# Optimization experiments

Measured on AMD Instinct MI355X. Metric: run time of the kernel, lower is better.

## Reference

```python
import jax, jax.numpy as jnp
import numpy as np

EPS = 1e-6

def rmsnorm(x, w):
    return x * jax.lax.rsqrt(jnp.mean(x * x, axis=-1, keepdims=True) + EPS) * w

def hard_sigmoid(x):
    # relu6(x + 3) / 6 - 0.5
    return jnp.clip(x + 3.0, 0.0, 6.0) / 6.0 - 0.5

def setup_inputs() -> dict:
    key = jax.random.key(0)
    ks = jax.random.split(key, 8)
    B, T, C, E = 4, 4096, 1024, 4
    H = E * C
    x = jax.random.normal(ks[0], (B, T, C), dtype=jnp.float32)
    norm1_w = jnp.ones((C,), dtype=jnp.float32)
    norm2_w = jnp.ones((C,), dtype=jnp.float32)
    s1 = 1.0 / np.sqrt(C)
    s2 = 1.0 / np.sqrt(H)
    mlp1_w = jax.random.uniform(ks[1], (C, C), jnp.float32, -s1, s1)
    mlp1_b = jax.random.uniform(ks[2], (C,), jnp.float32, -s1, s1)
    mlp2a_w = jax.random.uniform(ks[3], (C, H), jnp.float32, -s1, s1)
    mlp2a_b = jax.random.uniform(ks[4], (H,), jnp.float32, -s1, s1)
    mlp2b_w = jax.random.uniform(ks[5], (H, C), jnp.float32, -s2, s2)
    mlp2b_b = jax.random.uniform(ks[6], (C,), jnp.float32, -s2, s2)
    return {"x": x, "norm1_w": norm1_w, "mlp1_w": mlp1_w, "mlp1_b": mlp1_b,
            "norm2_w": norm2_w, "mlp2a_w": mlp2a_w, "mlp2a_b": mlp2a_b,
            "mlp2b_w": mlp2b_w, "mlp2b_b": mlp2b_b}

def reference(x, norm1_w, mlp1_w, mlp1_b, norm2_w, mlp2a_w, mlp2a_b, mlp2b_w, mlp2b_b):
    # state: [B, T, C] prefix sum over time of gated, normalized input
    state = jnp.cumsum(hard_sigmoid(rmsnorm(x, norm1_w)), axis=1)
    out = hard_sigmoid(state @ mlp1_w + mlp1_b) * x
    h = jax.nn.relu(rmsnorm(out, norm2_w) @ mlp2a_w + mlp2a_b)
    return h @ mlp2b_w + mlp2b_b + out
```

## Files before the change

kernel.cpp:

```cpp
#include <hip/hip_runtime.h>

#define B_     4
#define T_     4096
#define C_     1024
#define H_     4096
#define BT_    (B_ * T_)
#define NCH_   64
#define CHLEN_ 64
#define MCHUNK 8192

typedef __bf16 bf16_t;
typedef __bf16 bf16x8 __attribute__((ext_vector_type(8)));
typedef float  f32x4  __attribute__((ext_vector_type(4)));

__device__ __forceinline__ float hs_f(float v) {
    return fminf(fmaxf((v + 3.0f) * (1.0f / 6.0f), 0.0f), 1.0f) - 0.5f;
}

__device__ __forceinline__ void gld_lds16(const bf16_t* g, bf16_t* l) {
    __builtin_amdgcn_global_load_lds((const __attribute__((address_space(1))) void*)g,
                                     (__attribute__((address_space(3))) void*)l,
                                     16, 0, 0);
}

__global__ __launch_bounds__(256) void rms_rows_f32(const float* __restrict__ X,
                                                    float* __restrict__ inv) {
    const int wave = threadIdx.x >> 6, lane = threadIdx.x & 63;
    const int row = blockIdx.x * 4 + wave;
    const float* xr = X + (size_t)row * C_;
    float s = 0.0f;
    #pragma unroll
    for (int p = 0; p < 4; p++) {
        float4 v = *(const float4*)(xr + p * 256 + lane * 4);
        s += v.x * v.x + v.y * v.y + v.z * v.z + v.w * v.w;
    }
    #pragma unroll
    for (int o = 32; o > 0; o >>= 1) s += __shfl_down(s, o, 64);
    if (lane == 0) inv[row] = rsqrtf(s * (1.0f / C_) + 1e-6f);
}

__global__ __launch_bounds__(256) void rms_rows_bf16(const bf16_t* __restrict__ X,
                                                     float* __restrict__ inv) {
    const int wave = threadIdx.x >> 6, lane = threadIdx.x & 63;
    const int row = blockIdx.x * 4 + wave;
    const bf16_t* xr = X + (size_t)row * C_;
    bf16x8 v0 = *(const bf16x8*)(xr + lane * 8);
    bf16x8 v1 = *(const bf16x8*)(xr + 512 + lane * 8);
    float s = 0.0f;
    #pragma unroll
    for (int j = 0; j < 8; j++) {
        float a = (float)v0[j], b = (float)v1[j];
        s += a * a + b * b;
    }
    #pragma unroll
    for (int o = 32; o > 0; o >>= 1) s += __shfl_down(s, o, 64);
    if (lane == 0) inv[row] = rsqrtf(s * (1.0f / C_) + 1e-6f);
}

__global__ __launch_bounds__(256) void scan_emit_local(const float* __restrict__ X,
                                                       const float* __restrict__ inv1,
                                                       const float* __restrict__ nw,
                                                       bf16_t* __restrict__ state,
                                                       float* __restrict__ csum) {
    const int bch = blockIdx.x;
    const int b = bch >> 6, ch = bch & 63;
    const int c = blockIdx.y * 256 + threadIdx.x;
    const float wgt = nw[c];
    const int rbase = b * T_ + ch * CHLEN_;
    const size_t xbase = (size_t)rbase * C_ + c;
    float acc = 0.0f;
    for (int i = 0; i < CHLEN_; i++) {
        acc += hs_f(X[xbase + (size_t)i * C_] * inv1[rbase + i] * wgt);
        state[(size_t)(rbase + i) * C_ + c] = (bf16_t)acc;
    }
    csum[(size_t)bch * C_ + c] = acc;
}

__global__ __launch_bounds__(256) void scan_offsets_hilo(const float* __restrict__ csum,
                                                         bf16_t* __restrict__ hilo) {
    const int idx = blockIdx.x * 256 + threadIdx.x;
    const int b = idx >> 10, c = idx & 1023;
    const size_t base = (size_t)b * NCH_ * C_ + c;
    float v[NCH_];
    #pragma unroll
    for (int ch = 0; ch < NCH_; ch++)
        v[ch] = csum[base + (size_t)ch * C_];
    float run = 0.0f;
    #pragma unroll
    for (int ch = 0; ch < NCH_; ch++) {
        const size_t row = (size_t)(b * NCH_ + ch) * 2048 + c;
        const bf16_t hi = (bf16_t)run;
        hilo[row] = hi;
        hilo[row + 1024] = (bf16_t)(run - (float)hi);
        run += v[ch];
    }
}

__global__ __launch_bounds__(256) void pmat_init(const float* __restrict__ b1,
                                                 float* __restrict__ Pmat) {
    const int i = blockIdx.x * 256 + threadIdx.x;
    Pmat[i] = b1[i & (C_ - 1)];
}

__global__ __launch_bounds__(256) void transpose_scale(const float* __restrict__ src,
                                                       bf16_t* __restrict__ dst,
                                                       int K, int N, int ldd, int dupOff,
                                                       const float* __restrict__ scale) {
    __shared__ float tile[32][33];
    const int n0 = blockIdx.x * 32, k0 = blockIdx.y * 32;
    const int tx = threadIdx.x & 31, ty = threadIdx.x >> 5;
    #pragma unroll
    for (int j = 0; j < 4; j++) {
        const int kk = ty + j * 8;
        float v = src[(size_t)(k0 + kk) * N + n0 + tx];
        if (scale) v *= scale[k0 + kk];
        tile[kk][tx] = v;
    }
    __syncthreads();
    #pragma unroll
    for (int j = 0; j < 4; j++) {
        const int nn = ty + j * 8;
        const bf16_t v = (bf16_t)tile[tx][nn];
        dst[(size_t)(n0 + nn) * ldd + k0 + tx] = v;
        if (dupOff) dst[(size_t)(n0 + nn) * ldd + dupOff + k0 + tx] = v;
    }
}

template <int MODE, typename ET, typename OT>
__global__ __launch_bounds__(256) void gemm_bt(const bf16_t* __restrict__ A,
                                               const bf16_t* __restrict__ Bt,
                                               const float* __restrict__ bias,
                                               const ET* __restrict__ extra,
                                               const float* __restrict__ rowscale,
                                               const float* __restrict__ pmat,
                                               OT* __restrict__ Cmat,
                                               int N, int K, int lda, int ldb) {
    __shared__ __align__(16) bf16_t As[128 * 32];
    __shared__ __align__(16) bf16_t Bs[128 * 32];
    const int tid = threadIdx.x;

    const int nwgx = gridDim.x;
    const int flat0 = blockIdx.y * nwgx + blockIdx.x;
    int mTile, nTile;
    if ((nwgx & 7) == 0) {
        const int xcd = flat0 & 7;
        const int loc = flat0 >> 3;
        const int mpx = nwgx >> 3;
        mTile = xcd * mpx + (loc % mpx);
        nTile = loc / mpx;
    } else {
        mTile = blockIdx.x;
        nTile = blockIdx.y;
    }
    const int mBase = mTile * 128;
    const int nBase = nTile * 128;
    const size_t kOff = (size_t)blockIdx.z * K;

    const int wave = tid >> 6;
    const int lane = tid & 63;
    const int waveM = (wave & 1) * 64;
    const int waveN = (wave >> 1) * 64;
    const int lr = lane & 15;
    const int lq = lane >> 4;

    f32x4 acc[4][4] = {};

    const int e0 = tid * 8;
    const int r0 = e0 >> 5, c0 = e0 & 31;
    const int e1 = 2048 + tid * 8;
    const int r1 = e1 >> 5, c1 = e1 & 31;

    const bf16_t* Ag0 = A + (size_t)(mBase + r0) * lda + kOff + c0;
    const bf16_t* Ag1 = A + (size_t)(mBase + r1) * lda + kOff + c1;
    const bf16_t* Bg0 = Bt + (size_t)(nBase + r0) * ldb + kOff + c0;
    const bf16_t* Bg1 = Bt + (size_t)(nBase + r1) * ldb + kOff + c1;

    for (int kb = 0; kb < K; kb += 32) {
        __syncthreads();
        gld_lds16(Ag0 + kb, As + e0);
        gld_lds16(Ag1 + kb, As + e1);
        gld_lds16(Bg0 + kb, Bs + e0);
        gld_lds16(Bg1 + kb, Bs + e1);
        __syncthreads();

        bf16x8 af[4], bfr[4];
        #pragma unroll
        for (int mi = 0; mi < 4; mi++)
            af[mi] = *(const bf16x8*)(As + (waveM + mi * 16 + lr) * 32 + lq * 8);
        #pragma unroll
        for (int ni = 0; ni < 4; ni++)
            bfr[ni] = *(const bf16x8*)(Bs + (waveN + ni * 16 + lr) * 32 + lq * 8);
        #pragma unroll
        for (int mi = 0; mi < 4; mi++)
            #pragma unroll
            for (int ni = 0; ni < 4; ni++)
                acc[mi][ni] = __builtin_amdgcn_mfma_f32_16x16x32_bf16(
                    af[mi], bfr[ni], acc[mi][ni], 0, 0, 0);
    }

    #pragma unroll
    for (int ni = 0; ni < 4; ni++) {
        const int n = nBase + waveN + ni * 16 + lr;
        const float bz = (MODE == 1 || MODE == 2) ? bias[n] : 0.0f;
        #pragma unroll
        for (int mi = 0; mi < 4; mi++) {
            #pragma unroll
            for (int r = 0; r < 4; r++) {
                const int m = mBase + waveM + mi * 16 + lq * 4 + r;
                float v = acc[mi][ni][r];
                if (MODE == 0) {
                    v = hs_f(v + pmat[(size_t)(m >> 6) * N + n]) * (float)extra[(size_t)m * N + n];
                } else if (MODE == 1) {
                    v = fmaxf(rowscale[m] * v + bz, 0.0f);
                } else if (MODE == 2) {
                    v = v + bz + (float)extra[(size_t)m * N + n];
                }
                if (MODE == 4) {
                    atomicAdd((float*)&Cmat[(size_t)m * N + n], v);
                } else {
                    Cmat[(size_t)m * N + n] = (OT)v;
                }
            }
        }
    }
}

extern "C" void kernel_launch(void* const* d_in, const int* in_sizes, int n_in,
                              void* d_out, int out_size, void* d_ws, size_t ws_size,
                              hipStream_t stream) {
    const float* x   = (const float*)d_in[0];
    const float* n1w = (const float*)d_in[1];
    const float* w1  = (const float*)d_in[2];
    const float* b1  = (const float*)d_in[3];
    const float* n2w = (const float*)d_in[4];
    const float* w2a = (const float*)d_in[5];
    const float* b2a = (const float*)d_in[6];
    const float* w2b = (const float*)d_in[7];
    const float* b2b = (const float*)d_in[8];
    float* y = (float*)d_out;

    char* w = (char*)d_ws;
    float*  inv1  = (float*)(w + 0);
    float*  inv2  = (float*)(w + 65536);
    float*  csum  = (float*)(w + 131072);
    bf16_t* hilo  = (bf16_t*)(w + 1179648);
    float*  Pmat  = (float*)(w + 2228224);
    bf16_t* W1cat = (bf16_t*)(w + 5373952);
    bf16_t* W2at  = (bf16_t*)(w + 9568256);
    bf16_t* W2bt  = (bf16_t*)(w + 17956864);
    bf16_t* outb  = (bf16_t*)(w + 26345472);
    bf16_t* state = (bf16_t*)(w + 59899904);
    bf16_t* hbuf  = state;

    rms_rows_f32<<<dim3(BT_ / 4), dim3(256), 0, stream>>>(x, inv1);
    scan_emit_local<<<dim3(B_ * NCH_, C_ / 256), dim3(256), 0, stream>>>(x, inv1, n1w, state, csum);
    scan_offsets_hilo<<<dim3(B_ * C_ / 256), dim3(256), 0, stream>>>(csum, hilo);
    transpose_scale<<<dim3(C_ / 32, C_ / 32), dim3(256), 0, stream>>>(
        w1, W1cat, C_, C_, 2048, 1024, nullptr);
    transpose_scale<<<dim3(H_ / 32, C_ / 32), dim3(256), 0, stream>>>(
        w2a, W2at, C_, H_, C_, 0, n2w);
    transpose_scale<<<dim3(C_ / 32, H_ / 32), dim3(256), 0, stream>>>(
        w2b, W2bt, H_, C_, H_, 0, nullptr);
    pmat_init<<<dim3(256 * C_ / 256), dim3(256), 0, stream>>>(b1, Pmat);
    gemm_bt<4, float, float><<<dim3(2, C_ / 128, 4), dim3(256), 0, stream>>>(
        hilo, W1cat, nullptr, nullptr, nullptr, nullptr, Pmat, C_, 512, 2048, 2048);
    gemm_bt<0, float, bf16_t><<<dim3(BT_ / 128, C_ / 128), dim3(256), 0, stream>>>(
        state, W1cat, nullptr, x, nullptr, Pmat, outb, C_, C_, C_, 2048);
    rms_rows_bf16<<<dim3(BT_ / 4), dim3(256), 0, stream>>>(outb, inv2);
    for (int c = 0; c < BT_ / MCHUNK; c++) {
        const bf16_t* Ao = outb + (size_t)c * MCHUNK * C_;
        float* yo = y + (size_t)c * MCHUNK * C_;
        gemm_bt<1, float, bf16_t><<<dim3(MCHUNK / 128, H_ / 128), dim3(256), 0, stream>>>(
            Ao, W2at, b2a, nullptr, inv2 + c * MCHUNK, nullptr, hbuf, H_, C_, C_, C_);
        gemm_bt<2, bf16_t, float><<<dim3(MCHUNK / 128, C_ / 128), dim3(256), 0, stream>>>(
            hbuf, W2bt, b2b, Ao, nullptr, nullptr, yo, C_, H_, H_, H_);
    }
}
```

Before: 686.7 us.

## Replace 128x128 GEMM with pipelined 256x256 tile kernel using swizzled LDS

Moves the three large GEMMs to a new 256x256 tile kernel with 512 threads. It uses a K-step of 64, double-buffered LDS staging with global_load_lds, XOR swizzling against bank conflicts, interleaved prefetch with vmcnt waits, and s_setprio around MFMA bursts. The split-K atomic GEMM is kept as a separate simple kernel. The intent is more data reuse per tile and overlap of loads with MFMA work, at the cost of higher LDS and register use and fewer workgroups.

Measured after the change: 788.3 us. 1.15x slower.

```diff
diff --git a/kernel.cpp b/kernel.cpp
--- a/kernel.cpp
+++ b/kernel.cpp
@@ -126,18 +126,90 @@
     }
 }
 
-template <int MODE, typename ET, typename OT>
-__global__ __launch_bounds__(256) void gemm_bt(const bf16_t* __restrict__ A,
+__global__ __launch_bounds__(256) void gemm_pk(const bf16_t* __restrict__ A,
                                                const bf16_t* __restrict__ Bt,
-                                               const float* __restrict__ bias,
-                                               const ET* __restrict__ extra,
-                                               const float* __restrict__ rowscale,
-                                               const float* __restrict__ pmat,
-                                               OT* __restrict__ Cmat,
+                                               float* __restrict__ Cmat,
                                                int N, int K, int lda, int ldb) {
     __shared__ __align__(16) bf16_t As[128 * 32];
     __shared__ __align__(16) bf16_t Bs[128 * 32];
     const int tid = threadIdx.x;
+    const int mBase = blockIdx.x * 128;
+    const int nBase = blockIdx.y * 128;
+    const size_t kOff = (size_t)blockIdx.z * K;
+
+    const int wave = tid >> 6;
+    const int lane = tid & 63;
+    const int waveM = (wave & 1) * 64;
+    const int waveN = (wave >> 1) * 64;
+    const int lr = lane & 15;
+    const int lq = lane >> 4;
+
+    f32x4 acc[4][4] = {};
+
+    const int e0 = tid * 8;
+    const int r0 = e0 >> 5, c0 = e0 & 31;
+    const int e1 = 2048 + tid * 8;
+    const int r1 = e1 >> 5, c1 = e1 & 31;
+
+    const bf16_t* Ag0 = A + (size_t)(mBase + r0) * lda + kOff + c0;
+    const bf16_t* Ag1 = A + (size_t)(mBase + r1) * lda + kOff + c1;
+    const bf16_t* Bg0 = Bt + (size_t)(nBase + r0) * ldb + kOff + c0;
+    const bf16_t* Bg1 = Bt + (size_t)(nBase + r1) * ldb + kOff + c1;
+
+    for (int kb = 0; kb < K; kb += 32) {
+        __syncthreads();
+        gld_lds16(Ag0 + kb, As + e0);
+        gld_lds16(Ag1 + kb, As + e1);
+        gld_lds16(Bg0 + kb, Bs + e0);
+        gld_lds16(Bg1 + kb, Bs + e1);
+        __syncthreads();
+
+        bf16x8 af[4], bfr[4];
+        #pragma unroll
+        for (int mi = 0; mi < 4; mi++)
+            af[mi] = *(const bf16x8*)(As + (waveM + mi * 16 + lr) * 32 + lq * 8);
+        #pragma unroll
+        for (int ni = 0; ni < 4; ni++)
+            bfr[ni] = *(const bf16x8*)(Bs + (waveN + ni * 16 + lr) * 32 + lq * 8);
+        #pragma unroll
+        for (int mi = 0; mi < 4; mi++)
+            #pragma unroll
+            for (int ni = 0; ni < 4; ni++)
+                acc[mi][ni] = __builtin_amdgcn_mfma_f32_16x16x32_bf16(
+                    af[mi], bfr[ni], acc[mi][ni], 0, 0, 0);
+    }
+
+    #pragma unroll
+    for (int ni = 0; ni < 4; ni++) {
+        const int n = nBase + waveN + ni * 16 + lr;
+        #pragma unroll
+        for (int mi = 0; mi < 4; mi++) {
+            #pragma unroll
+            for (int r = 0; r < 4; r++) {
+                const int m = mBase + waveM + mi * 16 + lq * 4 + r;
+                atomicAdd(&Cmat[(size_t)m * N + n], acc[mi][ni][r]);
+            }
+        }
+    }
+}
+
+template <int MODE, typename ET, typename OT>
+__global__ __launch_bounds__(512, 2) void gemm256(const bf16_t* __restrict__ A,
+                                                  const bf16_t* __restrict__ Bt,
+                                                  const float* __restrict__ bias,
+                                                  const ET* __restrict__ extra,
+                                                  const float* __restrict__ rowscale,
+                                                  const float* __restrict__ pmat,
+                                                  OT* __restrict__ Cmat,
+                                                  int N, int K, int lda, int ldb) {
+    __shared__ __align__(16) bf16_t lds[2][2][256 * 64];
+
+    const int tid = threadIdx.x;
+    const int wave = tid >> 6, lane = tid & 63;
+    const int wm = wave >> 2;
+    const int wn = wave & 3;
+    const int lr = lane & 15;
+    const int lq = lane >> 4;
 
     const int nwgx = gridDim.x;
     const int flat0 = blockIdx.y * nwgx + blockIdx.x;
@@ -152,62 +224,109 @@
         mTile = blockIdx.x;
         nTile = blockIdx.y;
     }
-    const int mBase = mTile * 128;
-    const int nBase = nTile * 128;
-    const size_t kOff = (size_t)blockIdx.z * K;
-
-    const int wave = tid >> 6;
-    const int lane = tid & 63;
-    const int waveM = (wave & 1) * 64;
-    const int waveN = (wave >> 1) * 64;
-    const int lr = lane & 15;
-    const int lq = lane >> 4;
-
-    f32x4 acc[4][4] = {};
-
-    const int e0 = tid * 8;
-    const int r0 = e0 >> 5, c0 = e0 & 31;
-    const int e1 = 2048 + tid * 8;
-    const int r1 = e1 >> 5, c1 = e1 & 31;
-
-    const bf16_t* Ag0 = A + (size_t)(mBase + r0) * lda + kOff + c0;
-    const bf16_t* Ag1 = A + (size_t)(mBase + r1) * lda + kOff + c1;
-    const bf16_t* Bg0 = Bt + (size_t)(nBase + r0) * ldb + kOff + c0;
-    const bf16_t* Bg1 = Bt + (size_t)(nBase + r1) * ldb + kOff + c1;
-
-    for (int kb = 0; kb < K; kb += 32) {
-        __syncthreads();
-        gld_lds16(Ag0 + kb, As + e0);
-        gld_lds16(Ag1 + kb, As + e1);
-        gld_lds16(Bg0 + kb, Bs + e0);
-        gld_lds16(Bg1 + kb, Bs + e1);
-        __syncthreads();
-
-        bf16x8 af[4], bfr[4];
-        #pragma unroll
-        for (int mi = 0; mi < 4; mi++)
-            af[mi] = *(const bf16x8*)(As + (waveM + mi * 16 + lr) * 32 + lq * 8);
-        #pragma unroll
-        for (int ni = 0; ni < 4; ni++)
-            bfr[ni] = *(const bf16x8*)(Bs + (waveN + ni * 16 + lr) * 32 + lq * 8);
-        #pragma unroll
-        for (int mi = 0; mi < 4; mi++)
-            #pragma unroll
-            for (int ni = 0; ni < 4; ni++)
-                acc[mi][ni] = __builtin_amdgcn_mfma_f32_16x16x32_bf16(
-                    af[mi], bfr[ni], acc[mi][ni], 0, 0, 0);
-    }
-
-    #pragma unroll
-    for (int ni = 0; ni < 4; ni++) {
-        const int n = nBase + waveN + ni * 16 + lr;
+    const int mBase = mTile * 256;
+    const int nBase = nTile * 256;
+
+    const bf16_t* Abase = A + (size_t)mBase * lda;
+    const bf16_t* Bbase = Bt + (size_t)nBase * ldb;
+
+    auto stage = [&](int buf, int arr, int odd, int kb) {
+        #pragma unroll
+        for (int j = 0; j < 2; j++) {
+            const int ps = tid + (j << 9);
+            const int s  = ps & 7;
+            const int q  = ps >> 3;
+            int row;
+            if (arr == 0) row = ((q >> 6) << 7) | (odd << 6) | (q & 63);
+            else          row = ((q >> 5) << 6) | (odd << 5) | (q & 31);
+            const int c = (s ^ (row & 7)) << 3;
+            const bf16_t* src = (arr == 0 ? Abase + (size_t)row * lda
+                                          : Bbase + (size_t)row * ldb) + kb + c;
+            gld_lds16(src, &lds[buf][arr][row * 64 + s * 8]);
+        }
+    };
+
+    f32x4 acc[8][4] = {};
+
+    stage(0, 0, 0, 0); stage(0, 1, 0, 0); stage(0, 0, 1, 0); stage(0, 1, 1, 0);
+    stage(1, 0, 0, 64); stage(1, 1, 0, 64);
+    asm volatile("s_waitcnt vmcnt(4)" ::: "memory");
+    __builtin_amdgcn_s_barrier();
+
+    const int NIT = K >> 7;
+    for (int it = 0; it < NIT; ++it) {
+        const bool nl = (it + 1 < NIT);
+        const int k1 = ((it << 1) + 1) << 6;
+        const int k2 = ((it << 1) + 2) << 6;
+        const int k3 = ((it << 1) + 3) << 6;
+
+        #pragma unroll
+        for (int p = 0; p < 8; ++p) {
+            const int buf = p >> 2;
+            const int mh = (p >> 1) & 1, nh = p & 1;
+            const bf16_t* At = &lds[buf][0][0];
+            const bf16_t* Bl = &lds[buf][1][0];
+
+            bf16x8 af[4][2], bfr[2][2];
+            #pragma unroll
+            for (int mi = 0; mi < 4; mi++) {
+                const int R = wm * 128 + mh * 64 + mi * 16 + lr;
+                const size_t rb = (size_t)R * 64;
+                #pragma unroll
+                for (int ks = 0; ks < 2; ks++)
+                    af[mi][ks] = *(const bf16x8*)(At + rb + ((((ks << 2) | lq) ^ (R & 7)) << 3));
+            }
+            #pragma unroll
+            for (int ni = 0; ni < 2; ni++) {
+                const int R = wn * 64 + nh * 32 + ni * 16 + lr;
+                const size_t rb = (size_t)R * 64;
+                #pragma unroll
+                for (int ks = 0; ks < 2; ks++)
+                    bfr[ni][ks] = *(const bf16x8*)(Bl + rb + ((((ks << 2) | lq) ^ (R & 7)) << 3));
+            }
+
+            switch (p) {
+                case 0: stage(1, 0, 1, k1); break;
+                case 1: stage(1, 1, 1, k1); break;
+                case 2: if (nl) stage(0, 0, 0, k2); break;
+                case 3: if (nl) stage(0, 1, 0, k2); break;
+                case 4: if (nl) stage(0, 0, 1, k2); break;
+                case 5: if (nl) stage(0, 1, 1, k2); break;
+                case 6: if (nl) stage(1, 0, 0, k3); break;
+                case 7: if (nl) stage(1, 1, 0, k3); break;
+            }
+            if (p == 3) {
+                if (nl) asm volatile("s_waitcnt vmcnt(4)" ::: "memory");
+                else    asm volatile("s_waitcnt vmcnt(0)" ::: "memory");
+            }
+            if (p == 7 && nl) asm volatile("s_waitcnt vmcnt(4)" ::: "memory");
+
+            __builtin_amdgcn_s_barrier();
+            __builtin_amdgcn_s_setprio(1);
+            #pragma unroll
+            for (int mi = 0; mi < 4; mi++)
+                #pragma unroll
+                for (int ni = 0; ni < 2; ni++) {
+                    acc[mh * 4 + mi][nh * 2 + ni] = __builtin_amdgcn_mfma_f32_16x16x32_bf16(
+                        af[mi][0], bfr[ni][0], acc[mh * 4 + mi][nh * 2 + ni], 0, 0, 0);
+                    acc[mh * 4 + mi][nh * 2 + ni] = __builtin_amdgcn_mfma_f32_16x16x32_bf16(
+                        af[mi][1], bfr[ni][1], acc[mh * 4 + mi][nh * 2 + ni], 0, 0, 0);
+                }
+            __builtin_amdgcn_s_setprio(0);
+            __builtin_amdgcn_s_barrier();
+        }
+    }
+
+    #pragma unroll
+    for (int fn = 0; fn < 4; fn++) {
+        const int n = nBase + wn * 64 + fn * 16 + lr;
         const float bz = (MODE == 1 || MODE == 2) ? bias[n] : 0.0f;
         #pragma unroll
-        for (int mi = 0; mi < 4; mi++) {
+        for (int fm = 0; fm < 8; fm++) {
             #pragma unroll
             for (int r = 0; r < 4; r++) {
-                const int m = mBase + waveM + mi * 16 + lq * 4 + r;
-                float v = acc[mi][ni][r];
+                const int m = mBase + wm * 128 + fm * 16 + lq * 4 + r;
+                float v = acc[fm][fn][r];
                 if (MODE == 0) {
                     v = hs_f(v + pmat[(size_t)(m >> 6) * N + n]) * (float)extra[(size_t)m * N + n];
                 } else if (MODE == 1) {
@@ -215,11 +334,7 @@
                 } else if (MODE == 2) {
                     v = v + bz + (float)extra[(size_t)m * N + n];
                 }
-                if (MODE == 4) {
-                    atomicAdd((float*)&Cmat[(size_t)m * N + n], v);
-                } else {
-                    Cmat[(size_t)m * N + n] = (OT)v;
-                }
+                Cmat[(size_t)m * N + n] = (OT)v;
             }
         }
     }
@@ -262,17 +377,17 @@
     transpose_scale<<<dim3(C_ / 32, H_ / 32), dim3(256), 0, stream>>>(
         w2b, W2bt, H_, C_, H_, 0, nullptr);
     pmat_init<<<dim3(256 * C_ / 256), dim3(256), 0, stream>>>(b1, Pmat);
-    gemm_bt<4, float, float><<<dim3(2, C_ / 128, 4), dim3(256), 0, stream>>>(
-        hilo, W1cat, nullptr, nullptr, nullptr, nullptr, Pmat, C_, 512, 2048, 2048);
-    gemm_bt<0, float, bf16_t><<<dim3(BT_ / 128, C_ / 128), dim3(256), 0, stream>>>(
+    gemm_pk<<<dim3(2, C_ / 128, 4), dim3(256), 0, stream>>>(
+        hilo, W1cat, Pmat, C_, 512, 2048, 2048);
+    gemm256<0, float, bf16_t><<<dim3(BT_ / 256, C_ / 256), dim3(512), 0, stream>>>(
         state, W1cat, nullptr, x, nullptr, Pmat, outb, C_, C_, C_, 2048);
     rms_rows_bf16<<<dim3(BT_ / 4), dim3(256), 0, stream>>>(outb, inv2);
     for (int c = 0; c < BT_ / MCHUNK; c++) {
         const bf16_t* Ao = outb + (size_t)c * MCHUNK * C_;
         float* yo = y + (size_t)c * MCHUNK * C_;
-        gemm_bt<1, float, bf16_t><<<dim3(MCHUNK / 128, H_ / 128), dim3(256), 0, stream>>>(
+        gemm256<1, float, bf16_t><<<dim3(MCHUNK / 256, H_ / 256), dim3(512), 0, stream>>>(
             Ao, W2at, b2a, nullptr, inv2 + c * MCHUNK, nullptr, hbuf, H_, C_, C_, C_);
-        gemm_bt<2, bf16_t, float><<<dim3(MCHUNK / 128, C_ / 128), dim3(256), 0, stream>>>(
+        gemm256<2, bf16_t, float><<<dim3(MCHUNK / 256, C_ / 256), dim3(512), 0, stream>>>(
             hbuf, W2bt, b2b, Ao, nullptr, nullptr, yo, C_, H_, H_, H_);
     }
 }
```

## Double-buffer LDS tiles with async prefetch and XOR-swizzle the LDS layout

Applied to the files above, without the earlier changes.

The GEMM main loop now uses two LDS buffers per operand. The global-to-LDS loads for the tile two steps ahead are issued while MFMAs run on the current tile, and a partial `s_waitcnt vmcnt` replaces the full sync before each step. The k-chunk layout inside each LDS row is XOR-swizzled by row, applied on the global source address and undone on the fragment reads, to cut LDS bank conflicts on the bf16x8 fragment reads. This doubles LDS use per block, which may lower occupancy. The epilogue is also reorganised so every mode other than 0, 1 and 2 takes the atomicAdd path.

Result: faster. 607.2 us (-11.6%).

```diff
diff --git a/kernel.cpp b/kernel.cpp
--- a/kernel.cpp
+++ b/kernel.cpp
@@ -135,8 +135,8 @@
                                                const float* __restrict__ pmat,
                                                OT* __restrict__ Cmat,
                                                int N, int K, int lda, int ldb) {
-    __shared__ __align__(16) bf16_t As[128 * 32];
-    __shared__ __align__(16) bf16_t Bs[128 * 32];
+    __shared__ __align__(16) bf16_t As[2][128 * 32];
+    __shared__ __align__(16) bf16_t Bs[2][128 * 32];
     const int tid = threadIdx.x;
 
     const int nwgx = gridDim.x;
@@ -166,36 +166,52 @@
     f32x4 acc[4][4] = {};
 
     const int e0 = tid * 8;
-    const int r0 = e0 >> 5, c0 = e0 & 31;
+    const int r0 = e0 >> 5, c0 = (((e0 >> 3) & 3) ^ ((r0 >> 1) & 3)) << 3;
     const int e1 = 2048 + tid * 8;
-    const int r1 = e1 >> 5, c1 = e1 & 31;
+    const int r1 = e1 >> 5, c1 = (((e1 >> 3) & 3) ^ ((r1 >> 1) & 3)) << 3;
 
     const bf16_t* Ag0 = A + (size_t)(mBase + r0) * lda + kOff + c0;
     const bf16_t* Ag1 = A + (size_t)(mBase + r1) * lda + kOff + c1;
     const bf16_t* Bg0 = Bt + (size_t)(nBase + r0) * ldb + kOff + c0;
     const bf16_t* Bg1 = Bt + (size_t)(nBase + r1) * ldb + kOff + c1;
 
+    auto stage = [&](int buf, int kb) {
+        gld_lds16(Ag0 + kb, As[buf] + e0);
+        gld_lds16(Ag1 + kb, As[buf] + e1);
+        gld_lds16(Bg0 + kb, Bs[buf] + e0);
+        gld_lds16(Bg1 + kb, Bs[buf] + e1);
+    };
+
+    stage(0, 0);
+    if (32 < K) stage(1, 32);
+
+    int cur = 0;
     for (int kb = 0; kb < K; kb += 32) {
-        __syncthreads();
-        gld_lds16(Ag0 + kb, As + e0);
-        gld_lds16(Ag1 + kb, As + e1);
-        gld_lds16(Bg0 + kb, Bs + e0);
-        gld_lds16(Bg1 + kb, Bs + e1);
-        __syncthreads();
+        if (kb + 32 < K) asm volatile("s_waitcnt vmcnt(4)" ::: "memory");
+        else             asm volatile("s_waitcnt vmcnt(0)" ::: "memory");
+        __builtin_amdgcn_s_barrier();
 
         bf16x8 af[4], bfr[4];
         #pragma unroll
-        for (int mi = 0; mi < 4; mi++)
-            af[mi] = *(const bf16x8*)(As + (waveM + mi * 16 + lr) * 32 + lq * 8);
-        #pragma unroll
-        for (int ni = 0; ni < 4; ni++)
-            bfr[ni] = *(const bf16x8*)(Bs + (waveN + ni * 16 + lr) * 32 + lq * 8);
+        for (int mi = 0; mi < 4; mi++) {
+            const int R = waveM + mi * 16 + lr;
+            af[mi] = *(const bf16x8*)(As[cur] + R * 32 + ((lq ^ ((R >> 1) & 3)) << 3));
+        }
+        #pragma unroll
+        for (int ni = 0; ni < 4; ni++) {
+            const int R = waveN + ni * 16 + lr;
+            bfr[ni] = *(const bf16x8*)(Bs[cur] + R * 32 + ((lq ^ ((R >> 1) & 3)) << 3));
+        }
         #pragma unroll
         for (int mi = 0; mi < 4; mi++)
             #pragma unroll
             for (int ni = 0; ni < 4; ni++)
                 acc[mi][ni] = __builtin_amdgcn_mfma_f32_16x16x32_bf16(
                     af[mi], bfr[ni], acc[mi][ni], 0, 0, 0);
+
+        __builtin_amdgcn_s_barrier();
+        if (kb + 64 < K) stage(cur, kb + 64);
+        cur ^= 1;
     }
 
     #pragma unroll
@@ -210,15 +226,15 @@
                 float v = acc[mi][ni][r];
                 if (MODE == 0) {
                     v = hs_f(v + pmat[(size_t)(m >> 6) * N + n]) * (float)extra[(size_t)m * N + n];
+                    Cmat[(size_t)m * N + n] = (OT)v;
                 } else if (MODE == 1) {
                     v = fmaxf(rowscale[m] * v + bz, 0.0f);
+                    Cmat[(size_t)m * N + n] = (OT)v;
                 } else if (MODE == 2) {
                     v = v + bz + (float)extra[(size_t)m * N + n];
-                }
-                if (MODE == 4) {
+                    Cmat[(size_t)m * N + n] = (OT)v;
+                } else {
                     atomicAdd((float*)&Cmat[(size_t)m * N + n], v);
-                } else {
-                    Cmat[(size_t)m * N + n] = (OT)v;
                 }
             }
         }
```
